# Kernel tuning notes

Measured on AMD Instinct MI355X. Metric: run time of the kernel, lower is better.

Reference implementation:

```python
import jax, jax.numpy as jnp
import numpy as np

S = 14
L_COORD = 5.0
L_NOOBJ = 0.5


def setup_inputs() -> dict:
    key = jax.random.key(0)
    k1, k2, k3, k4 = jax.random.split(key, 4)
    N = 4096
    # positive uniforms so sqrt(w), sqrt(h) and IoU areas are well-defined (as in real YOLO outputs)
    pred_tensor = jax.random.uniform(k1, (N, S, S, 30), dtype=jnp.float32, minval=0.01, maxval=1.0)
    target_boxes = jax.random.uniform(k2, (N, S, S, 4), dtype=jnp.float32, minval=0.01, maxval=1.0)
    target_cls = jax.random.uniform(k3, (N, S, S, 20), dtype=jnp.float32)
    has_object_map = jax.random.bernoulli(k4, 0.15, (N, S, S))
    return {"pred_tensor": pred_tensor, "target_boxes": target_boxes,
            "target_cls": target_cls, "has_object_map": has_object_map}


def _xywh2xyxy(b):
    # b: (..., 4) as [cx, cy, w, h]; cx,cy are in grid units -> divide by S
    x, y, w, h = b[..., 0], b[..., 1], b[..., 2], b[..., 3]
    return jnp.stack([x / S - 0.5 * w, y / S - 0.5 * h,
                      x / S + 0.5 * w, y / S + 0.5 * h], axis=-1)


def _iou_pairwise(b1, b2):
    # elementwise IoU between matched boxes (diag of compute_iou), b: (..., 4) xyxy
    lt = jnp.maximum(b1[..., :2], b2[..., :2])
    rb = jnp.minimum(b1[..., 2:], b2[..., 2:])
    wh = jnp.maximum(rb - lt, 0.0)
    inter = wh[..., 0] * wh[..., 1]
    a1 = (b1[..., 2] - b1[..., 0]) * (b1[..., 3] - b1[..., 1])
    a2 = (b2[..., 2] - b2[..., 0]) * (b2[..., 3] - b2[..., 1])
    return inter / (a1 + a2 - inter)


def reference(pred_tensor, target_boxes, target_cls, has_object_map):
    N = pred_tensor.shape[0]
    obj = has_object_map.astype(pred_tensor.dtype)          # (N,S,S)
    noobj = 1.0 - obj

    box1 = pred_tensor[..., 0:5]
    box2 = pred_tensor[..., 5:10]
    pred_cls = pred_tensor[..., 10:]

    # class loss: masked sum-MSE over object cells
    cls_loss = jnp.sum(obj[..., None] * (pred_cls - target_cls) ** 2)

    # no-object loss: confidences of both predictors in non-object cells vs 0
    no_obj_loss = L_NOOBJ * jnp.sum(noobj * (box1[..., 4] ** 2 + box2[..., 4] ** 2))

    # best-of-B selection by IoU against target (elementwise, matched per cell)
    tgt_xyxy = _xywh2xyxy(target_boxes)
    iou1 = _iou_pairwise(_xywh2xyxy(box1[..., :4]), tgt_xyxy)
    iou2 = _iou_pairwise(_xywh2xyxy(box2[..., :4]), tgt_xyxy)
    take1 = iou1 > iou2
    best_iou = jnp.where(take1, iou1, iou2)                  # (N,S,S)
    best_box = jnp.where(take1[..., None], box1, box2)       # (N,S,S,5)

    xy_err = jnp.sum((best_box[..., :2] - target_boxes[..., :2]) ** 2, axis=-1)
    wh_err = jnp.sum((jnp.sqrt(best_box[..., 2:4]) - jnp.sqrt(target_boxes[..., 2:4])) ** 2, axis=-1)
    reg_loss = L_COORD * jnp.sum(obj * (xy_err + wh_err))

    # containing-object confidence loss; target IoU is detached
    contain_loss = jnp.sum(obj * (best_box[..., 4] - jax.lax.stop_gradient(best_iou)) ** 2)

    total = cls_loss + no_obj_loss + contain_loss + reg_loss
    # [total, reg, containing_obj, no_obj, cls], each averaged over batch
    return jnp.stack([total, reg_loss, contain_loss, no_obj_loss, cls_loss]) / N
```

## Files before the change

### kernel.cpp

```cpp
#include <hip/hip_runtime.h>


#define NBATCH   4096
#define CELLS    (NBATCH * 14 * 14)
#define THREADS  256
#define NBLK     2048
#define NWAVES   (NBLK * 4)
#define CHUNKS   (CELLS / 32)
#define L_COORD  5.0f
#define L_NOOBJ  0.5f

__global__ __launch_bounds__(THREADS, 8) void yolo_main(
    const float* __restrict__ pred,
    const float* __restrict__ tbox,
    const float* __restrict__ tcls,
    const int*   __restrict__ objmap,
    float4*      __restrict__ part)
{
    __shared__ float lds[4 * 960];
    __shared__ float red[4][4];

    const int tid  = threadIdx.x;
    const int wv   = tid >> 6;
    const int lane = tid & 63;
    float* seg = &lds[wv * 960];

    const int i1  = lane + 64, i2 = lane + 128;
    const int cc0 = lane / 5;
    const int cc1 = i1 / 5;
    const int cc2 = (lane < 32) ? (i2 / 5) : 0;
    const int ch0a = (lane - cc0 * 5) * 4;
    const int ch0b = (i1   - cc1 * 5) * 4;
    const int ch0c = (i2   - cc2 * 5) * 4;
    const int bcell = lane >> 1;
    const int box   = lane & 1;
    const float invS = 1.0f / 14.0f;

    float acc_reg = 0.f, acc_cont = 0.f, acc_noobj = 0.f, acc_cls = 0.f;

    const int gw0 = blockIdx.x * 4 + wv;
    for (int chunk = gw0; chunk < CHUNKS; chunk += NWAVES) {
        const size_t cbase = (size_t)chunk * 32;

        const int* ob = objmap + cbase;
        const int o0  = ob[cc0];
        const int o1  = ob[cc1];
        const int o2  = ob[cc2];
        const int obx = ob[bcell];
        const float4 tb = ((const float4*)tbox)[cbase + bcell];

        const float4* p4 = (const float4*)pred + (size_t)chunk * 240;
        float4* s4 = (float4*)seg;
        float4 v0 = p4[lane];
        float4 v1 = p4[i1];
        float4 v2 = p4[i2];
        float4 v3;
        if (lane < 48) v3 = p4[lane + 192];
        s4[lane] = v0;
        s4[i1]   = v1;
        s4[i2]   = v2;
        if (lane < 48) s4[lane + 192] = v3;

        __builtin_amdgcn_s_waitcnt(0);

        {
            const float4* t4 = (const float4*)tcls + (size_t)chunk * 160;
            float cl = 0.f;
            if (o0) {
                float4 t = t4[lane];
                const float* pc = &seg[cc0 * 30 + 10 + ch0a];
                float d0 = pc[0]-t.x, d1 = pc[1]-t.y, d2 = pc[2]-t.z, d3 = pc[3]-t.w;
                cl += d0*d0 + d1*d1 + d2*d2 + d3*d3;
            }
            if (o1) {
                float4 t = t4[i1];
                const float* pc = &seg[cc1 * 30 + 10 + ch0b];
                float d0 = pc[0]-t.x, d1 = pc[1]-t.y, d2 = pc[2]-t.z, d3 = pc[3]-t.w;
                cl += d0*d0 + d1*d1 + d2*d2 + d3*d3;
            }
            if ((lane < 32) && o2) {
                float4 t = t4[i2];
                const float* pc = &seg[cc2 * 30 + 10 + ch0c];
                float d0 = pc[0]-t.x, d1 = pc[1]-t.y, d2 = pc[2]-t.z, d3 = pc[3]-t.w;
                cl += d0*d0 + d1*d1 + d2*d2 + d3*d3;
            }
            acc_cls += cl;
        }

        {
            const float* pp = &seg[bcell * 30 + box * 5];
            float x = pp[0], y = pp[1], w = pp[2], h = pp[3], conf = pp[4];

            if (!obx) acc_noobj += conf * conf;

            float txc = tb.x * invS, tyc = tb.y * invS;
            float tx1 = txc - 0.5f * tb.z, ty1 = tyc - 0.5f * tb.w;
            float tx2 = txc + 0.5f * tb.z, ty2 = tyc + 0.5f * tb.w;
            float ta  = (tx2 - tx1) * (ty2 - ty1);

            float ax1 = x * invS - 0.5f * w, ay1 = y * invS - 0.5f * h;
            float ax2 = x * invS + 0.5f * w, ay2 = y * invS + 0.5f * h;
            float a1  = (ax2 - ax1) * (ay2 - ay1);
            float iw  = fmaxf(fminf(ax2, tx2) - fmaxf(ax1, tx1), 0.f);
            float ih  = fmaxf(fminf(ay2, ty2) - fmaxf(ay1, ty1), 0.f);
            float inter = iw * ih;
            float iou   = inter / (a1 + ta - inter);

            float iou_other = __shfl_xor(iou, 1);
            bool win = (box == 0) ? (iou > iou_other) : !(iou_other > iou);

            if (win && obx) {
                float dx = x - tb.x, dy = y - tb.y;
                float dw = sqrtf(w) - sqrtf(tb.z);
                float dh = sqrtf(h) - sqrtf(tb.w);
                acc_reg  += dx*dx + dy*dy + dw*dw + dh*dh;
                float dc  = conf - iou;
                acc_cont += dc * dc;
            }
        }
    }

    #pragma unroll
    for (int off = 32; off > 0; off >>= 1) {
        acc_reg   += __shfl_down(acc_reg,   off);
        acc_cont  += __shfl_down(acc_cont,  off);
        acc_noobj += __shfl_down(acc_noobj, off);
        acc_cls   += __shfl_down(acc_cls,   off);
    }
    if (lane == 0) {
        red[wv][0] = acc_reg;
        red[wv][1] = acc_cont;
        red[wv][2] = acc_noobj;
        red[wv][3] = acc_cls;
    }
    __syncthreads();
    if (tid == 0) {
        float4 p;
        p.x = red[0][0] + red[1][0] + red[2][0] + red[3][0];
        p.y = red[0][1] + red[1][1] + red[2][1] + red[3][1];
        p.z = red[0][2] + red[1][2] + red[2][2] + red[3][2];
        p.w = red[0][3] + red[1][3] + red[2][3] + red[3][3];
        part[blockIdx.x] = p;
    }
}

__global__ __launch_bounds__(1024) void yolo_reduce(
    const float4* __restrict__ part, float* __restrict__ out)
{
    __shared__ float red[16][4];
    float r = 0.f, c = 0.f, n = 0.f, cl = 0.f;
    #pragma unroll
    for (int i = threadIdx.x; i < NBLK; i += 1024) {
        float4 p = part[i];
        r += p.x; c += p.y; n += p.z; cl += p.w;
    }
    #pragma unroll
    for (int off = 32; off > 0; off >>= 1) {
        r  += __shfl_down(r,  off);
        c  += __shfl_down(c,  off);
        n  += __shfl_down(n,  off);
        cl += __shfl_down(cl, off);
    }
    const int wave = threadIdx.x >> 6, lane = threadIdx.x & 63;
    if (lane == 0) {
        red[wave][0] = r; red[wave][1] = c; red[wave][2] = n; red[wave][3] = cl;
    }
    __syncthreads();
    if (threadIdx.x == 0) {
        float R = 0.f, C = 0.f, Nn = 0.f, Cl = 0.f;
        #pragma unroll
        for (int w = 0; w < 16; ++w) {
            R += red[w][0]; C += red[w][1]; Nn += red[w][2]; Cl += red[w][3];
        }
        const float invN = 1.0f / (float)NBATCH;
        float reg   = L_COORD * R  * invN;
        float cont  =           C  * invN;
        float noobj = L_NOOBJ * Nn * invN;
        float cls   =           Cl * invN;
        out[0] = reg + cont + noobj + cls;
        out[1] = reg;
        out[2] = cont;
        out[3] = noobj;
        out[4] = cls;
    }
}

extern "C" void kernel_launch(void* const* d_in, const int* in_sizes, int n_in,
                              void* d_out, int out_size, void* d_ws, size_t ws_size,
                              hipStream_t stream) {
    const float* pred   = (const float*)d_in[0];
    const float* tbox   = (const float*)d_in[1];
    const float* tcls   = (const float*)d_in[2];
    const int*   objmap = (const int*)  d_in[3];
    float4* part = (float4*)d_ws;
    float*  out  = (float*)d_out;

    yolo_main<<<NBLK, THREADS, 0, stream>>>(pred, tbox, tcls, objmap, part);
    yolo_reduce<<<1, 1024, 0, stream>>>(part, out);
}
```

Baseline: 195.7 us.

## Software-pipeline next-chunk loads into registers and shuffle objmap across lanes

The main loop now prefetches the next chunk's pred, target-box and objmap data into registers while the current chunk is processed, double-buffering through registers instead of stalling on a full waitcnt. Objmap is loaded once per lane (32 ints) and distributed with __shfl rather than four separate global loads. The target-class loads are issued before the IoU work to overlap their latency. Grid size and occupancy hint drop from 8 to 6 blocks per CU to make room for the extra registers, at the cost of fewer resident waves to hide latency.

```diff
diff --git a/kernel.cpp b/kernel.cpp
--- a/kernel.cpp
+++ b/kernel.cpp
@@ -4,13 +4,13 @@
 #define NBATCH   4096
 #define CELLS    (NBATCH * 14 * 14)
 #define THREADS  256
-#define NBLK     2048
+#define NBLK     1536
 #define NWAVES   (NBLK * 4)
 #define CHUNKS   (CELLS / 32)
 #define L_COORD  5.0f
 #define L_NOOBJ  0.5f
 
-__global__ __launch_bounds__(THREADS, 8) void yolo_main(
+__global__ __launch_bounds__(THREADS, 6) void yolo_main(
     const float* __restrict__ pred,
     const float* __restrict__ tbox,
     const float* __restrict__ tcls,
@@ -24,6 +24,7 @@
     const int wv   = tid >> 6;
     const int lane = tid & 63;
     float* seg = &lds[wv * 960];
+    float4* s4 = (float4*)seg;
 
     const int i1  = lane + 64, i2 = lane + 128;
     const int cc0 = lane / 5;
@@ -34,58 +35,62 @@
     const int ch0c = (i2   - cc2 * 5) * 4;
     const int bcell = lane >> 1;
     const int box   = lane & 1;
+    const int l31   = lane & 31;
     const float invS = 1.0f / 14.0f;
 
     float acc_reg = 0.f, acc_cont = 0.f, acc_noobj = 0.f, acc_cls = 0.f;
 
     const int gw0 = blockIdx.x * 4 + wv;
-    for (int chunk = gw0; chunk < CHUNKS; chunk += NWAVES) {
-        const size_t cbase = (size_t)chunk * 32;
-
-        const int* ob = objmap + cbase;
-        const int o0  = ob[cc0];
-        const int o1  = ob[cc1];
-        const int o2  = ob[cc2];
-        const int obx = ob[bcell];
-        const float4 tb = ((const float4*)tbox)[cbase + bcell];
-
-        const float4* p4 = (const float4*)pred + (size_t)chunk * 240;
-        float4* s4 = (float4*)seg;
-        float4 v0 = p4[lane];
-        float4 v1 = p4[i1];
-        float4 v2 = p4[i2];
-        float4 v3;
-        if (lane < 48) v3 = p4[lane + 192];
-        s4[lane] = v0;
-        s4[i1]   = v1;
-        s4[i2]   = v2;
-        if (lane < 48) s4[lane + 192] = v3;
-
-        __builtin_amdgcn_s_waitcnt(0);
-
-        {
-            const float4* t4 = (const float4*)tcls + (size_t)chunk * 160;
-            float cl = 0.f;
-            if (o0) {
-                float4 t = t4[lane];
-                const float* pc = &seg[cc0 * 30 + 10 + ch0a];
-                float d0 = pc[0]-t.x, d1 = pc[1]-t.y, d2 = pc[2]-t.z, d3 = pc[3]-t.w;
-                cl += d0*d0 + d1*d1 + d2*d2 + d3*d3;
-            }
-            if (o1) {
-                float4 t = t4[i1];
-                const float* pc = &seg[cc1 * 30 + 10 + ch0b];
-                float d0 = pc[0]-t.x, d1 = pc[1]-t.y, d2 = pc[2]-t.z, d3 = pc[3]-t.w;
-                cl += d0*d0 + d1*d1 + d2*d2 + d3*d3;
-            }
-            if ((lane < 32) && o2) {
-                float4 t = t4[i2];
-                const float* pc = &seg[cc2 * 30 + 10 + ch0c];
-                float d0 = pc[0]-t.x, d1 = pc[1]-t.y, d2 = pc[2]-t.z, d3 = pc[3]-t.w;
-                cl += d0*d0 + d1*d1 + d2*d2 + d3*d3;
-            }
-            acc_cls += cl;
-        }
+
+    float4 pv0, pv1, pv2, pv3;
+    float4 tbv;
+    int    ov;
+    {
+        const size_t cb = (size_t)gw0 * 32;
+        const float4* p4 = (const float4*)pred + (size_t)gw0 * 240;
+        ov  = objmap[cb + l31];
+        tbv = ((const float4*)tbox)[cb + bcell];
+        pv0 = p4[lane];
+        pv1 = p4[i1];
+        pv2 = p4[i2];
+        if (lane < 48) pv3 = p4[lane + 192];
+    }
+
+    for (int c = gw0; c < CHUNKS; c += NWAVES) {
+        float4 a0 = pv0, a1 = pv1, a2 = pv2, a3 = pv3;
+        float4 tb = tbv;
+        int    ob = ov;
+
+        const int cn = c + NWAVES;
+        if (cn < CHUNKS) {
+            const size_t cb = (size_t)cn * 32;
+            const float4* p4 = (const float4*)pred + (size_t)cn * 240;
+            ov  = objmap[cb + l31];
+            tbv = ((const float4*)tbox)[cb + bcell];
+            pv0 = p4[lane];
+            pv1 = p4[i1];
+            pv2 = p4[i2];
+            if (lane < 48) pv3 = p4[lane + 192];
+        }
+
+        s4[lane] = a0;
+        s4[i1]   = a1;
+        s4[i2]   = a2;
+        if (lane < 48) s4[lane + 192] = a3;
+
+        const int o0  = __shfl(ob, cc0);
+        const int o1  = __shfl(ob, cc1);
+        const int o2  = __shfl(ob, cc2);
+        const int obx = __shfl(ob, bcell);
+
+        float4 t0, t1, t2;
+        const float4* t4 = (const float4*)tcls + (size_t)c * 160;
+        const bool g0 = (o0 != 0);
+        const bool g1 = (o1 != 0);
+        const bool g2 = (lane < 32) && (o2 != 0);
+        if (g0) t0 = t4[lane];
+        if (g1) t1 = t4[i1];
+        if (g2) t2 = t4[i2];
 
         {
             const float* pp = &seg[bcell * 30 + box * 5];
@@ -100,11 +105,11 @@
 
             float ax1 = x * invS - 0.5f * w, ay1 = y * invS - 0.5f * h;
             float ax2 = x * invS + 0.5f * w, ay2 = y * invS + 0.5f * h;
-            float a1  = (ax2 - ax1) * (ay2 - ay1);
+            float a1b = (ax2 - ax1) * (ay2 - ay1);
             float iw  = fmaxf(fminf(ax2, tx2) - fmaxf(ax1, tx1), 0.f);
             float ih  = fmaxf(fminf(ay2, ty2) - fmaxf(ay1, ty1), 0.f);
             float inter = iw * ih;
-            float iou   = inter / (a1 + ta - inter);
+            float iou   = inter / (a1b + ta - inter);
 
             float iou_other = __shfl_xor(iou, 1);
             bool win = (box == 0) ? (iou > iou_other) : !(iou_other > iou);
@@ -117,6 +122,26 @@
                 float dc  = conf - iou;
                 acc_cont += dc * dc;
             }
+        }
+
+        {
+            float cl = 0.f;
+            if (g0) {
+                const float* pc = &seg[cc0 * 30 + 10 + ch0a];
+                float d0 = pc[0]-t0.x, d1 = pc[1]-t0.y, d2 = pc[2]-t0.z, d3 = pc[3]-t0.w;
+                cl += d0*d0 + d1*d1 + d2*d2 + d3*d3;
+            }
+            if (g1) {
+                const float* pc = &seg[cc1 * 30 + 10 + ch0b];
+                float d0 = pc[0]-t1.x, d1 = pc[1]-t1.y, d2 = pc[2]-t1.z, d3 = pc[3]-t1.w;
+                cl += d0*d0 + d1*d1 + d2*d2 + d3*d3;
+            }
+            if (g2) {
+                const float* pc = &seg[cc2 * 30 + 10 + ch0c];
+                float d0 = pc[0]-t2.x, d1 = pc[1]-t2.y, d2 = pc[2]-t2.z, d3 = pc[3]-t2.w;
+                cl += d0*d0 + d1*d1 + d2*d2 + d3*d3;
+            }
+            acc_cls += cl;
         }
     }
 
@@ -149,7 +174,6 @@
 {
     __shared__ float red[16][4];
     float r = 0.f, c = 0.f, n = 0.f, cl = 0.f;
-    #pragma unroll
     for (int i = threadIdx.x; i < NBLK; i += 1024) {
         float4 p = part[i];
         r += p.x; c += p.y; n += p.z; cl += p.w;
```

Result: slower. 202.5 us (+3.5%).
